# Optimization experiments

Hardware: AMD Instinct MI355X
Metric: run time of the kernel (lower is better)

The kernel has to match this reference:

```python
import jax, jax.numpy as jnp
import numpy as np

NEG_BIG = -9e15
ALPHA = 0.2  # leakyrelu negative slope


def setup_inputs() -> dict:
    key = jax.random.key(0)
    k1, k2, k3, k4 = jax.random.split(key, 4)
    N, F_in, F_out = 8192, 256, 256
    h = jax.random.normal(k1, (N, F_in), dtype=jnp.float32)
    adj = jax.random.randint(k2, (N, N), 0, 2).astype(jnp.float32)
    W = jax.random.normal(k3, (F_in, F_out), dtype=jnp.float32) * (1.414 / np.sqrt(F_in))
    a = jax.random.normal(k4, (2 * F_out, 1), dtype=jnp.float32) * (1.414 / np.sqrt(2 * F_out))
    return {"h": h, "adj": adj, "W": W, "a": a}


def reference(h, adj, W, a):
    F_out = W.shape[1]
    Wh = h @ W  # [N, F_out]
    # Decomposed additive score: e_ij = leakyrelu(a1.Wh_i + a2.Wh_j)
    # identical to matmul(cat([Wh_i, Wh_j]), a) in the original.
    a1 = a[:F_out, 0]  # [F_out]
    a2 = a[F_out:, 0]  # [F_out]
    s1 = Wh @ a1  # [N]
    s2 = Wh @ a2  # [N]
    e = jax.nn.leaky_relu(s1[:, None] + s2[None, :], negative_slope=ALPHA)  # [N, N]
    e = jnp.where(adj > 0, e, NEG_BIG)
    attention = jax.nn.softmax(e, axis=1)
    # dropout skipped (eval mode: training=False)
    h_prime = attention @ Wh  # [N, F_out]
    return jax.nn.elu(h_prime)
```

## Files before the change

### kernel.cpp

```cpp
#include <hip/hip_runtime.h>
#include <hip/hip_bf16.h>

#define N 8192
#define F 256
#define KSPLIT 8
#define JBLK (N / KSPLIT)
#define NITER (JBLK / 64)
#define LOG2E 1.4426950408889634f

using s16x8 = __attribute__((ext_vector_type(8))) short;
using f32x4 = __attribute__((ext_vector_type(4))) float;

static __device__ __forceinline__ unsigned short f2bf(float f) {
  unsigned int u = __float_as_uint(f);
  unsigned int r = u + 0x7fffu + ((u >> 16) & 1u);
  return (unsigned short)(r >> 16);
}
static __device__ __forceinline__ float bf2f(unsigned short u) {
  return __uint_as_float(((unsigned int)u) << 16);
}
static __device__ __forceinline__ void glds16(const char* g, char* l) {
  __builtin_amdgcn_global_load_lds(
      (const __attribute__((address_space(1))) unsigned int*)g,
      (__attribute__((address_space(3))) unsigned int*)l, 16, 0, 0);
}

__global__ __launch_bounds__(256) void k_mask(const float* __restrict__ adj,
                                              unsigned int* __restrict__ mask) {
  __shared__ unsigned int nibw[8192];
  int t = threadIdx.x;
  for (int s = 0; s < 4; ++s) {
    size_t chunk = (size_t)s * 2048 + blockIdx.x;
    const float* base = adj + chunk * 8192;
    unsigned int nib[8];
#pragma unroll
    for (int r = 0; r < 8; ++r) {
      float4 v = *reinterpret_cast<const float4*>(base + (size_t)(r * 256 + t) * 4);
      nib[r] = (v.x != 0.f ? 1u : 0u) | (v.y != 0.f ? 2u : 0u) |
               (v.z != 0.f ? 4u : 0u) | (v.w != 0.f ? 8u : 0u);
    }
    if (s) __syncthreads();
#pragma unroll
    for (int r = 0; r < 8; ++r) nibw[r * 256 + t] = nib[r];
    __syncthreads();
    unsigned int wrd = 0;
#pragma unroll
    for (int k = 0; k < 8; ++k) wrd |= nibw[t * 8 + k] << (4 * k);
    mask[chunk * 256 + t] = wrd;
  }
}

__global__ __launch_bounds__(256) void k0_wt(const float* __restrict__ W,
                                             unsigned short* __restrict__ Wt) {
  int k = blockIdx.x;
  int f = threadIdx.x;
  Wt[f * 256 + k] = f2bf(W[k * 256 + f]);
}

__global__ __launch_bounds__(256) void k1_wh(const float* __restrict__ h,
                                             const unsigned short* __restrict__ Wt,
                                             const float* __restrict__ a,
                                             char* __restrict__ WhbT,
                                             float* __restrict__ s1g,
                                             float* __restrict__ s2g) {
  __shared__ char lds[8192 + 32768];
  char* Alds = lds;
  char* Blds = lds + 8192;
  int t = threadIdx.x;
  int i0 = blockIdx.x * 64;
  int l = t & 63, w = t >> 6;
  int lr = l & 15, lk = l >> 4;
  f32x4 acc[4][4] = {};
  for (int kt = 0; kt < 4; ++kt) {
    int k0 = kt * 64;
    if (kt) __syncthreads();
#pragma unroll
    for (int c = 0; c < 4; ++c) {
      int flat = c * 256 + t;
      int i = flat >> 4, jc = flat & 15;
      float4 v = *reinterpret_cast<const float4*>(h + (size_t)(i0 + i) * 256 + k0 + jc * 4);
      ushort4 pk;
      pk.x = f2bf(v.x); pk.y = f2bf(v.y); pk.z = f2bf(v.z); pk.w = f2bf(v.w);
      *reinterpret_cast<ushort4*>(Alds + i * 128 + ((jc * 8) ^ ((i & 7) << 4))) = pk;
    }
#pragma unroll
    for (int c = 0; c < 8; ++c) {
      int idx = c * 256 + t;
      int fr = idx >> 3, kc = idx & 7;
      uint4 v = *reinterpret_cast<const uint4*>(Wt + fr * 256 + k0 + kc * 8);
      *reinterpret_cast<uint4*>(Blds + fr * 128 + ((kc * 16) ^ ((fr & 7) << 4))) = v;
    }
    __syncthreads();
#pragma unroll
    for (int kk = 0; kk < 2; ++kk) {
      int kofs = kk * 64 + lk * 16;
      s16x8 afr[4], bfr[4];
#pragma unroll
      for (int mf = 0; mf < 4; ++mf) {
        int ar = mf * 16 + lr;
        afr[mf] = *reinterpret_cast<const s16x8*>(Alds + ar * 128 + (kofs ^ ((ar & 7) << 4)));
      }
#pragma unroll
      for (int nf = 0; nf < 4; ++nf) {
        int br = w * 64 + nf * 16 + lr;
        bfr[nf] = *reinterpret_cast<const s16x8*>(Blds + br * 128 + (kofs ^ ((br & 7) << 4)));
      }
#pragma unroll
      for (int mf = 0; mf < 4; ++mf)
#pragma unroll
        for (int nf = 0; nf < 4; ++nf)
          acc[mf][nf] = __builtin_amdgcn_mfma_f32_16x16x32_bf16(afr[mf], bfr[nf], acc[mf][nf], 0, 0, 0);
    }
  }
  int tj = blockIdx.x;
#pragma unroll
  for (int mf = 0; mf < 4; ++mf) {
#pragma unroll
    for (int nf = 0; nf < 4; ++nf) {
      int f = w * 64 + nf * 16 + lr;
      int jj = mf * 16 + lk * 4;
      int kc = jj >> 3, sub = (jj >> 2) & 1;
      ushort4 pk;
      pk.x = f2bf(acc[mf][nf][0]);
      pk.y = f2bf(acc[mf][nf][1]);
      pk.z = f2bf(acc[mf][nf][2]);
      pk.w = f2bf(acc[mf][nf][3]);
      *reinterpret_cast<ushort4*>(WhbT + (size_t)tj * 32768 + f * 128 +
                                  ((kc * 16) ^ ((f & 7) << 4)) + sub * 8) = pk;
    }
  }
  float a1v[4], a2v[4];
#pragma unroll
  for (int nf = 0; nf < 4; ++nf) {
    int f = w * 64 + nf * 16 + lr;
    a1v[nf] = a[f];
    a2v[nf] = a[256 + f];
  }
  float* s1l = (float*)lds;
  float* s2l = s1l + 64;
  __syncthreads();
  if (t < 128) s1l[t] = 0.f;
  __syncthreads();
#pragma unroll
  for (int mf = 0; mf < 4; ++mf) {
#pragma unroll
    for (int r = 0; r < 4; ++r) {
      float p1 = 0.f, p2 = 0.f;
#pragma unroll
      for (int nf = 0; nf < 4; ++nf) {
        p1 += acc[mf][nf][r] * a1v[nf];
        p2 += acc[mf][nf][r] * a2v[nf];
      }
      p1 += __shfl_xor(p1, 1); p1 += __shfl_xor(p1, 2);
      p1 += __shfl_xor(p1, 4); p1 += __shfl_xor(p1, 8);
      p2 += __shfl_xor(p2, 1); p2 += __shfl_xor(p2, 2);
      p2 += __shfl_xor(p2, 4); p2 += __shfl_xor(p2, 8);
      if (lr == 0) {
        atomicAdd(&s1l[mf * 16 + lk * 4 + r], p1);
        atomicAdd(&s2l[mf * 16 + lk * 4 + r], p2);
      }
    }
  }
  __syncthreads();
  if (t < 64) {
    s1g[i0 + t] = s1l[t] * LOG2E;
    s2g[i0 + t] = s2l[t] * LOG2E;
  }
}

__global__ __launch_bounds__(256, 2) void k3_attn(const unsigned char* __restrict__ mask8,
                                                  const char* __restrict__ WhbT,
                                                  const float* __restrict__ s1,
                                                  const float* __restrict__ s2,
                                                  float* __restrict__ numw,
                                                  float* __restrict__ denw) {
  __shared__ char lds[2 * 32768 + 4096];
  char* Bbuf = lds;
  float* s2l = (float*)(lds + 65536);
  int t = threadIdx.x, w = t >> 6, l = t & 63, lr = l & 15, lk = l >> 4;
  int i0 = blockIdx.x * 128;
  int ks = blockIdx.y;
  int jb = ks * JBLK;

  {
    float4 v = *reinterpret_cast<const float4*>(s2 + jb + t * 4);
    *reinterpret_cast<float4*>(s2l + t * 4) = v;
  }
  int row0 = i0 + w * 32 + lr;
  int row1 = row0 + 16;
  float s1p0 = s1[row0], s1p1 = s1[row1];
  const unsigned char* mr0 = mask8 + (size_t)row0 * (N / 8) + (jb >> 3);
  const unsigned char* mr1 = mask8 + (size_t)row1 * (N / 8) + (jb >> 3);

  f32x4 acc[2][16] = {};
  float ds0 = 0.f, ds1 = 0.f;

#define GLDS_TILE(tile, buf)                                                  \
  {                                                                           \
    const char* gsrc = WhbT + ((size_t)(ks * NITER + (tile))) * 32768;        \
    char* ldst = Bbuf + (buf) * 32768;                                        \
    _Pragma("unroll") for (int c = 0; c < 8; ++c)                             \
        glds16(gsrc + c * 4096 + w * 1024 + l * 16, ldst + c * 4096 + w * 1024); \
  }

  unsigned int mb0a = mr0[lk], mb0b = mr0[4 + lk];
  unsigned int mb1a = mr1[lk], mb1b = mr1[4 + lk];
  GLDS_TILE(0, 0);

  for (int it = 0; it < NITER; ++it) {
    int cb = it & 1;
    bool pf = (it + 1) < NITER;
    unsigned int nb0a = 0, nb0b = 0, nb1a = 0, nb1b = 0;
    if (pf) {
      int o = (it + 1) * 8;
      nb0a = mr0[o + lk]; nb0b = mr0[o + 4 + lk];
      nb1a = mr1[o + lk]; nb1b = mr1[o + 4 + lk];
      GLDS_TILE(it + 1, cb ^ 1);
      asm volatile("s_waitcnt vmcnt(8)" ::: "memory");
    } else {
      asm volatile("s_waitcnt vmcnt(0)" ::: "memory");
    }
    asm volatile("s_waitcnt lgkmcnt(0)" ::: "memory");
    __builtin_amdgcn_s_barrier();

    s16x8 af00, af01, af10, af11;
    {
      int jofs = it * 64 + lk * 8;
      float4 sa0 = *reinterpret_cast<const float4*>(s2l + jofs);
      float4 sb0 = *reinterpret_cast<const float4*>(s2l + jofs + 4);
      float4 sa1 = *reinterpret_cast<const float4*>(s2l + jofs + 32);
      float4 sb1 = *reinterpret_cast<const float4*>(s2l + jofs + 36);
#define PEL(dst, e, s1p, sv, mv, dsx)                                         \
      {                                                                       \
        float x = (s1p) + (sv); x = fmaxf(x, 0.2f * x);                       \
        float p = ((mv >> (e)) & 1u) ? exp2f(x) : 0.f;                        \
        unsigned short us = (unsigned short)((__float_as_uint(p) + 0x8000u) >> 16); \
        dsx += bf2f(us); dst[e] = (short)us;                                  \
      }
#define PFRAG(dst, s1p, sa, sb, mv, dsx)                                      \
      PEL(dst, 0, s1p, sa.x, mv, dsx) PEL(dst, 1, s1p, sa.y, mv, dsx)         \
      PEL(dst, 2, s1p, sa.z, mv, dsx) PEL(dst, 3, s1p, sa.w, mv, dsx)         \
      PEL(dst, 4, s1p, sb.x, mv, dsx) PEL(dst, 5, s1p, sb.y, mv, dsx)         \
      PEL(dst, 6, s1p, sb.z, mv, dsx) PEL(dst, 7, s1p, sb.w, mv, dsx)
      PFRAG(af00, s1p0, sa0, sb0, mb0a, ds0)
      PFRAG(af01, s1p0, sa1, sb1, mb0b, ds0)
      PFRAG(af10, s1p1, sa0, sb0, mb1a, ds1)
      PFRAG(af11, s1p1, sa1, sb1, mb1b, ds1)
#undef PFRAG
#undef PEL
    }
    const char* B = Bbuf + cb * 32768;
#pragma unroll
    for (int kk = 0; kk < 2; ++kk) {
      int kofs = kk * 64 + lk * 16;
      s16x8 a0 = kk ? af01 : af00;
      s16x8 a1 = kk ? af11 : af10;
#pragma unroll
      for (int nf = 0; nf < 16; ++nf) {
        int br = nf * 16 + lr;
        s16x8 bfr = *reinterpret_cast<const s16x8*>(B + br * 128 + (kofs ^ ((br & 7) << 4)));
        acc[0][nf] = __builtin_amdgcn_mfma_f32_16x16x32_bf16(a0, bfr, acc[0][nf], 0, 0, 0);
        acc[1][nf] = __builtin_amdgcn_mfma_f32_16x16x32_bf16(a1, bfr, acc[1][nf], 0, 0, 0);
      }
    }
    asm volatile("s_waitcnt lgkmcnt(0)" ::: "memory");
    __builtin_amdgcn_s_barrier();
    mb0a = nb0a; mb0b = nb0b; mb1a = nb1a; mb1b = nb1b;
  }
#undef GLDS_TILE

  ds0 += __shfl_xor(ds0, 16); ds0 += __shfl_xor(ds0, 32);
  ds1 += __shfl_xor(ds1, 16); ds1 += __shfl_xor(ds1, 32);
  if (l < 16) {
    denw[(size_t)ks * N + row0] = ds0;
    denw[(size_t)ks * N + row1] = ds1;
  }
  float* nump = numw + (size_t)ks * N * F;
#pragma unroll
  for (int mf = 0; mf < 2; ++mf) {
#pragma unroll
    for (int nf = 0; nf < 16; ++nf) {
#pragma unroll
      for (int r = 0; r < 4; ++r) {
        nump[(size_t)(i0 + w * 32 + mf * 16 + lk * 4 + r) * F + nf * 16 + lr] = acc[mf][nf][r];
      }
    }
  }
}

__global__ __launch_bounds__(256) void k4_fin(const float* __restrict__ numw,
                                              const float* __restrict__ denw,
                                              float* __restrict__ out) {
  int idx = (blockIdx.x * 256 + threadIdx.x) * 4;
  int i = idx >> 8;
  float4 sn = {0.f, 0.f, 0.f, 0.f};
  float sd = 0.f;
#pragma unroll
  for (int ksp = 0; ksp < KSPLIT; ++ksp) {
    float4 v = *reinterpret_cast<const float4*>(numw + (size_t)ksp * N * F + idx);
    sn.x += v.x; sn.y += v.y; sn.z += v.z; sn.w += v.w;
    sd += denw[(size_t)ksp * N + i];
  }
  float r = 1.f / sd;
  float4 o;
  float hp;
  hp = sn.x * r; o.x = hp > 0.f ? hp : (__expf(hp) - 1.f);
  hp = sn.y * r; o.y = hp > 0.f ? hp : (__expf(hp) - 1.f);
  hp = sn.z * r; o.z = hp > 0.f ? hp : (__expf(hp) - 1.f);
  hp = sn.w * r; o.w = hp > 0.f ? hp : (__expf(hp) - 1.f);
  *reinterpret_cast<float4*>(out + idx) = o;
}

extern "C" void kernel_launch(void* const* d_in, const int* in_sizes, int n_in,
                              void* d_out, int out_size, void* d_ws, size_t ws_size,
                              hipStream_t stream) {
  const float* h   = (const float*)d_in[0];
  const float* adj = (const float*)d_in[1];
  const float* W   = (const float*)d_in[2];
  const float* a   = (const float*)d_in[3];
  float* out = (float*)d_out;

  char* ws = (char*)d_ws;
  size_t o = 0;
  char* WhbT           = ws + o;                        o += (size_t)4 * 1024 * 1024;
  float* s1            = (float*)(ws + o);              o += 32768;
  float* s2            = (float*)(ws + o);              o += 32768;
  float* denw          = (float*)(ws + o);              o += (size_t)KSPLIT * N * 4;
  unsigned short* Wt   = (unsigned short*)(ws + o);     o += 131072;
  unsigned int* mask   = (unsigned int*)(ws + o);       o += (size_t)N * (N / 32) * 4;
  float* numw          = (float*)(ws + o);              o += (size_t)KSPLIT * N * F * 4;

  hipLaunchKernelGGL(k_mask, dim3(2048), dim3(256), 0, stream, adj, mask);
  hipLaunchKernelGGL(k0_wt, dim3(256), dim3(256), 0, stream, W, Wt);
  hipLaunchKernelGGL(k1_wh, dim3(N / 64), dim3(256), 0, stream, h, Wt, a, WhbT, s1, s2);
  hipLaunchKernelGGL(k3_attn, dim3(N / 128, KSPLIT), dim3(256), 0, stream,
                     (const unsigned char*)mask, WhbT, s1, s2, numw, denw);
  hipLaunchKernelGGL(k4_fin, dim3(N * F / 1024), dim3(256), 0, stream, numw, denw, out);
}
```

Before: 155.2 us.

## Fuse adjacency masking into attention kernel and read Wh tiles directly from global

Removes the separate bitmask-packing kernel. The attention kernel now reads the fp32 adjacency rows directly with nontemporal loads, double-buffered in registers. The LDS double-buffered Wh tile staging and its barriers are dropped, and B fragments are loaded straight from global/L2. Tiles shrink to 64 rows per block, each wave owning 16 rows, and the K split drops from 8 to 4. This trades one fewer kernel and pass over the 256MB adj matrix for more L2 traffic on Wh, since each wave re-reads the B tile without LDS sharing.

```diff
diff --git a/kernel.cpp b/kernel.cpp
--- a/kernel.cpp
+++ b/kernel.cpp
@@ -3,7 +3,7 @@
 
 #define N 8192
 #define F 256
-#define KSPLIT 8
+#define KSPLIT 4
 #define JBLK (N / KSPLIT)
 #define NITER (JBLK / 64)
 #define LOG2E 1.4426950408889634f
@@ -19,35 +19,8 @@
 static __device__ __forceinline__ float bf2f(unsigned short u) {
   return __uint_as_float(((unsigned int)u) << 16);
 }
-static __device__ __forceinline__ void glds16(const char* g, char* l) {
-  __builtin_amdgcn_global_load_lds(
-      (const __attribute__((address_space(1))) unsigned int*)g,
-      (__attribute__((address_space(3))) unsigned int*)l, 16, 0, 0);
-}
-
-__global__ __launch_bounds__(256) void k_mask(const float* __restrict__ adj,
-                                              unsigned int* __restrict__ mask) {
-  __shared__ unsigned int nibw[8192];
-  int t = threadIdx.x;
-  for (int s = 0; s < 4; ++s) {
-    size_t chunk = (size_t)s * 2048 + blockIdx.x;
-    const float* base = adj + chunk * 8192;
-    unsigned int nib[8];
-#pragma unroll
-    for (int r = 0; r < 8; ++r) {
-      float4 v = *reinterpret_cast<const float4*>(base + (size_t)(r * 256 + t) * 4);
-      nib[r] = (v.x != 0.f ? 1u : 0u) | (v.y != 0.f ? 2u : 0u) |
-               (v.z != 0.f ? 4u : 0u) | (v.w != 0.f ? 8u : 0u);
-    }
-    if (s) __syncthreads();
-#pragma unroll
-    for (int r = 0; r < 8; ++r) nibw[r * 256 + t] = nib[r];
-    __syncthreads();
-    unsigned int wrd = 0;
-#pragma unroll
-    for (int k = 0; k < 8; ++k) wrd |= nibw[t * 8 + k] << (4 * k);
-    mask[chunk * 256 + t] = wrd;
-  }
+static __device__ __forceinline__ f32x4 ntl4(const float* p) {
+  return __builtin_nontemporal_load(reinterpret_cast<const f32x4*>(p));
 }
 
 __global__ __launch_bounds__(256) void k0_wt(const float* __restrict__ W,
@@ -168,122 +141,98 @@
   }
 }
 
-__global__ __launch_bounds__(256, 2) void k3_attn(const unsigned char* __restrict__ mask8,
-                                                  const char* __restrict__ WhbT,
-                                                  const float* __restrict__ s1,
-                                                  const float* __restrict__ s2,
-                                                  float* __restrict__ numw,
-                                                  float* __restrict__ denw) {
-  __shared__ char lds[2 * 32768 + 4096];
-  char* Bbuf = lds;
-  float* s2l = (float*)(lds + 65536);
+__global__ __launch_bounds__(256) void k3_attn(const float* __restrict__ adj,
+                                               const char* __restrict__ WhbT,
+                                               const float* __restrict__ s1,
+                                               const float* __restrict__ s2,
+                                               float* __restrict__ numw,
+                                               float* __restrict__ denw) {
+  __shared__ float s2l[JBLK];
   int t = threadIdx.x, w = t >> 6, l = t & 63, lr = l & 15, lk = l >> 4;
-  int i0 = blockIdx.x * 128;
+  int i0 = blockIdx.x * 64;
   int ks = blockIdx.y;
   int jb = ks * JBLK;
-
-  {
-    float4 v = *reinterpret_cast<const float4*>(s2 + jb + t * 4);
-    *reinterpret_cast<float4*>(s2l + t * 4) = v;
-  }
-  int row0 = i0 + w * 32 + lr;
-  int row1 = row0 + 16;
-  float s1p0 = s1[row0], s1p1 = s1[row1];
-  const unsigned char* mr0 = mask8 + (size_t)row0 * (N / 8) + (jb >> 3);
-  const unsigned char* mr1 = mask8 + (size_t)row1 * (N / 8) + (jb >> 3);
-
-  f32x4 acc[2][16] = {};
-  float ds0 = 0.f, ds1 = 0.f;
-
-#define GLDS_TILE(tile, buf)                                                  \
-  {                                                                           \
-    const char* gsrc = WhbT + ((size_t)(ks * NITER + (tile))) * 32768;        \
-    char* ldst = Bbuf + (buf) * 32768;                                        \
-    _Pragma("unroll") for (int c = 0; c < 8; ++c)                             \
-        glds16(gsrc + c * 4096 + w * 1024 + l * 16, ldst + c * 4096 + w * 1024); \
-  }
-
-  unsigned int mb0a = mr0[lk], mb0b = mr0[4 + lk];
-  unsigned int mb1a = mr1[lk], mb1b = mr1[4 + lk];
-  GLDS_TILE(0, 0);
-
-  for (int it = 0; it < NITER; ++it) {
-    int cb = it & 1;
-    bool pf = (it + 1) < NITER;
-    unsigned int nb0a = 0, nb0b = 0, nb1a = 0, nb1b = 0;
-    if (pf) {
-      int o = (it + 1) * 8;
-      nb0a = mr0[o + lk]; nb0b = mr0[o + 4 + lk];
-      nb1a = mr1[o + lk]; nb1b = mr1[o + 4 + lk];
-      GLDS_TILE(it + 1, cb ^ 1);
-      asm volatile("s_waitcnt vmcnt(8)" ::: "memory");
-    } else {
-      asm volatile("s_waitcnt vmcnt(0)" ::: "memory");
-    }
-    asm volatile("s_waitcnt lgkmcnt(0)" ::: "memory");
-    __builtin_amdgcn_s_barrier();
-
-    s16x8 af00, af01, af10, af11;
-    {
-      int jofs = it * 64 + lk * 8;
-      float4 sa0 = *reinterpret_cast<const float4*>(s2l + jofs);
-      float4 sb0 = *reinterpret_cast<const float4*>(s2l + jofs + 4);
-      float4 sa1 = *reinterpret_cast<const float4*>(s2l + jofs + 32);
-      float4 sb1 = *reinterpret_cast<const float4*>(s2l + jofs + 36);
-#define PEL(dst, e, s1p, sv, mv, dsx)                                         \
-      {                                                                       \
-        float x = (s1p) + (sv); x = fmaxf(x, 0.2f * x);                       \
-        float p = ((mv >> (e)) & 1u) ? exp2f(x) : 0.f;                        \
-        unsigned short us = (unsigned short)((__float_as_uint(p) + 0x8000u) >> 16); \
-        dsx += bf2f(us); dst[e] = (short)us;                                  \
-      }
-#define PFRAG(dst, s1p, sa, sb, mv, dsx)                                      \
-      PEL(dst, 0, s1p, sa.x, mv, dsx) PEL(dst, 1, s1p, sa.y, mv, dsx)         \
-      PEL(dst, 2, s1p, sa.z, mv, dsx) PEL(dst, 3, s1p, sa.w, mv, dsx)         \
-      PEL(dst, 4, s1p, sb.x, mv, dsx) PEL(dst, 5, s1p, sb.y, mv, dsx)         \
-      PEL(dst, 6, s1p, sb.z, mv, dsx) PEL(dst, 7, s1p, sb.w, mv, dsx)
-      PFRAG(af00, s1p0, sa0, sb0, mb0a, ds0)
-      PFRAG(af01, s1p0, sa1, sb1, mb0b, ds0)
-      PFRAG(af10, s1p1, sa0, sb0, mb1a, ds1)
-      PFRAG(af11, s1p1, sa1, sb1, mb1b, ds1)
+  int lko = lk * 8;
+
+  *reinterpret_cast<float4*>(&s2l[t * 8]) = *reinterpret_cast<const float4*>(s2 + jb + t * 8);
+  *reinterpret_cast<float4*>(&s2l[t * 8 + 4]) = *reinterpret_cast<const float4*>(s2 + jb + t * 8 + 4);
+
+  int row = i0 + w * 16 + lr;
+  const float* arow = adj + (size_t)row * N + jb;
+  float s1v = s1[row];
+
+  f32x4 acc[16] = {};
+  float ds = 0.f;
+  f32x4 ajA[4], ajB[4];
+
+#pragma unroll
+  for (int q = 0; q < 2; ++q) {
+    ajA[q]     = ntl4(arow + lko + q * 4);
+    ajA[2 + q] = ntl4(arow + 32 + lko + q * 4);
+  }
+  __syncthreads();
+
+#define PEL(dst, e, av, sv)                                                    \
+  {                                                                            \
+    float x = s1v + (sv); x = fmaxf(x, 0.2f * x);                              \
+    float p = (av) > 0.f ? exp2f(x) : 0.f;                                     \
+    unsigned short us = (unsigned short)((__float_as_uint(p) + 0x8000u) >> 16);\
+    ds += bf2f(us); dst[e] = (short)us;                                        \
+  }
+#define PFRAG(dst, a0, a1, sv0, sv1)                                           \
+  PEL(dst, 0, a0.x, sv0.x) PEL(dst, 1, a0.y, sv0.y)                            \
+  PEL(dst, 2, a0.z, sv0.z) PEL(dst, 3, a0.w, sv0.w)                            \
+  PEL(dst, 4, a1.x, sv1.x) PEL(dst, 5, a1.y, sv1.y)                            \
+  PEL(dst, 6, a1.z, sv1.z) PEL(dst, 7, a1.w, sv1.w)
+
+#define BODY(IT, CUR, NXT)                                                     \
+  {                                                                            \
+    const int it = (IT);                                                       \
+    float4 sa0 = *reinterpret_cast<const float4*>(&s2l[it * 64 + lko]);        \
+    float4 sb0 = *reinterpret_cast<const float4*>(&s2l[it * 64 + lko + 4]);    \
+    float4 sa1 = *reinterpret_cast<const float4*>(&s2l[it * 64 + 32 + lko]);   \
+    float4 sb1 = *reinterpret_cast<const float4*>(&s2l[it * 64 + 32 + lko + 4]);\
+    s16x8 af0, af1;                                                            \
+    PFRAG(af0, CUR[0], CUR[1], sa0, sb0)                                       \
+    PFRAG(af1, CUR[2], CUR[3], sa1, sb1)                                       \
+    const char* Bt = WhbT + (size_t)(ks * NITER + it) * 32768;                 \
+    _Pragma("unroll") for (int kk = 0; kk < 2; ++kk) {                         \
+      int kofs = kk * 64 + lk * 16;                                            \
+      s16x8 af = kk ? af1 : af0;                                               \
+      _Pragma("unroll") for (int nf = 0; nf < 16; ++nf) {                      \
+        int br = nf * 16 + lr;                                                 \
+        s16x8 bfr = *reinterpret_cast<const s16x8*>(                           \
+            Bt + br * 128 + (kofs ^ ((br & 7) << 4)));                         \
+        acc[nf] = __builtin_amdgcn_mfma_f32_16x16x32_bf16(af, bfr, acc[nf], 0, 0, 0); \
+      }                                                                        \
+    }                                                                          \
+    if (it + 1 < NITER) {                                                      \
+      const float* ap = arow + (it + 1) * 64;                                  \
+      _Pragma("unroll") for (int q = 0; q < 2; ++q) {                          \
+        NXT[q]     = ntl4(ap + lko + q * 4);                                   \
+        NXT[2 + q] = ntl4(ap + 32 + lko + q * 4);                              \
+      }                                                                        \
+    }                                                                          \
+  }
+
+  for (int it2 = 0; it2 < NITER / 2; ++it2) {
+    BODY(2 * it2, ajA, ajB);
+    BODY(2 * it2 + 1, ajB, ajA);
+  }
+#undef BODY
 #undef PFRAG
 #undef PEL
-    }
-    const char* B = Bbuf + cb * 32768;
-#pragma unroll
-    for (int kk = 0; kk < 2; ++kk) {
-      int kofs = kk * 64 + lk * 16;
-      s16x8 a0 = kk ? af01 : af00;
-      s16x8 a1 = kk ? af11 : af10;
-#pragma unroll
-      for (int nf = 0; nf < 16; ++nf) {
-        int br = nf * 16 + lr;
-        s16x8 bfr = *reinterpret_cast<const s16x8*>(B + br * 128 + (kofs ^ ((br & 7) << 4)));
-        acc[0][nf] = __builtin_amdgcn_mfma_f32_16x16x32_bf16(a0, bfr, acc[0][nf], 0, 0, 0);
-        acc[1][nf] = __builtin_amdgcn_mfma_f32_16x16x32_bf16(a1, bfr, acc[1][nf], 0, 0, 0);
-      }
-    }
-    asm volatile("s_waitcnt lgkmcnt(0)" ::: "memory");
-    __builtin_amdgcn_s_barrier();
-    mb0a = nb0a; mb0b = nb0b; mb1a = nb1a; mb1b = nb1b;
-  }
-#undef GLDS_TILE
-
-  ds0 += __shfl_xor(ds0, 16); ds0 += __shfl_xor(ds0, 32);
-  ds1 += __shfl_xor(ds1, 16); ds1 += __shfl_xor(ds1, 32);
-  if (l < 16) {
-    denw[(size_t)ks * N + row0] = ds0;
-    denw[(size_t)ks * N + row1] = ds1;
-  }
+
+  ds += __shfl_xor(ds, 16);
+  ds += __shfl_xor(ds, 32);
+  if (l < 16) denw[(size_t)ks * N + row] = ds;
+
   float* nump = numw + (size_t)ks * N * F;
 #pragma unroll
-  for (int mf = 0; mf < 2; ++mf) {
-#pragma unroll
-    for (int nf = 0; nf < 16; ++nf) {
-#pragma unroll
-      for (int r = 0; r < 4; ++r) {
-        nump[(size_t)(i0 + w * 32 + mf * 16 + lk * 4 + r) * F + nf * 16 + lr] = acc[mf][nf][r];
-      }
+  for (int nf = 0; nf < 16; ++nf) {
+#pragma unroll
+    for (int r = 0; r < 4; ++r) {
+      nump[(size_t)(i0 + w * 16 + lk * 4 + r) * F + nf * 16 + lr] = acc[nf][r];
     }
   }
 }
@@ -322,18 +271,16 @@
 
   char* ws = (char*)d_ws;
   size_t o = 0;
-  char* WhbT           = ws + o;                        o += (size_t)4 * 1024 * 1024;
-  float* s1            = (float*)(ws + o);              o += 32768;
-  float* s2            = (float*)(ws + o);              o += 32768;
-  float* denw          = (float*)(ws + o);              o += (size_t)KSPLIT * N * 4;
-  unsigned short* Wt   = (unsigned short*)(ws + o);     o += 131072;
-  unsigned int* mask   = (unsigned int*)(ws + o);       o += (size_t)N * (N / 32) * 4;
-  float* numw          = (float*)(ws + o);              o += (size_t)KSPLIT * N * F * 4;
-
-  hipLaunchKernelGGL(k_mask, dim3(2048), dim3(256), 0, stream, adj, mask);
+  char* WhbT           = ws + o;                    o += (size_t)4 * 1024 * 1024;
+  float* s1            = (float*)(ws + o);          o += 32768;
+  float* s2            = (float*)(ws + o);          o += 32768;
+  float* denw          = (float*)(ws + o);          o += (size_t)KSPLIT * N * 4;
+  unsigned short* Wt   = (unsigned short*)(ws + o); o += 131072;
+  float* numw          = (float*)(ws + o);          o += (size_t)KSPLIT * N * F * 4;
+
   hipLaunchKernelGGL(k0_wt, dim3(256), dim3(256), 0, stream, W, Wt);
   hipLaunchKernelGGL(k1_wh, dim3(N / 64), dim3(256), 0, stream, h, Wt, a, WhbT, s1, s2);
-  hipLaunchKernelGGL(k3_attn, dim3(N / 128, KSPLIT), dim3(256), 0, stream,
-                     (const unsigned char*)mask, WhbT, s1, s2, numw, denw);
+  hipLaunchKernelGGL(k3_attn, dim3(N / 64, KSPLIT), dim3(256), 0, stream,
+                     adj, WhbT, s1, s2, numw, denw);
   hipLaunchKernelGGL(k4_fin, dim3(N * F / 1024), dim3(256), 0, stream, numw, denw, out);
 }
```

Measured after the change: 299.9 us. 1.93x slower.
